# Kernel tuning notes

Measured on AMD Instinct MI355X. Metric: run time of the kernel, lower is better.

## Reference

```python
import jax, jax.numpy as jnp
import numpy as np

D_MODEL = 1024
NUM_HEADS = 16
HEAD_DIM = D_MODEL // NUM_HEADS  # 64
M_BITS = 32
B, N = 4, 2048


def setup_inputs() -> dict:
    key = jax.random.key(0)
    ks = jax.random.split(key, 6)
    s = 1.0 / np.sqrt(D_MODEL)
    se = 1.0 / np.sqrt(HEAD_DIM)
    return {
        "x": jax.random.normal(ks[0], (B, N, D_MODEL), dtype=jnp.float32),
        "Wq": jax.random.normal(ks[1], (D_MODEL, D_MODEL), dtype=jnp.float32) * s,
        "Wk": jax.random.normal(ks[2], (D_MODEL, D_MODEL), dtype=jnp.float32) * s,
        "Wv": jax.random.normal(ks[3], (D_MODEL, D_MODEL), dtype=jnp.float32) * s,
        # per-head witness (bit) encoders: project head_dim -> m_bits
        "W_enc": jax.random.normal(ks[4], (NUM_HEADS, HEAD_DIM, M_BITS), dtype=jnp.float32) * se,
        "Wo": jax.random.normal(ks[5], (D_MODEL, D_MODEL), dtype=jnp.float32) * s,
    }


def reference(x, Wq, Wk, Wv, W_enc, Wo):
    Bsz, Nq, _ = x.shape
    # QKV projections (nn.Linear, no bias): y = x @ W^T
    Q = x @ Wq.T
    K = x @ Wk.T  # self-attention: context = x
    V = x @ Wv.T
    # split heads: [B, N, H, hd]
    Qh = Q.reshape(Bsz, Nq, NUM_HEADS, HEAD_DIM)
    Kh = K.reshape(Bsz, Nq, NUM_HEADS, HEAD_DIM)
    Vh = V.reshape(Bsz, Nq, NUM_HEADS, HEAD_DIM)
    # witness encodings: soft-bit (tanh of random-hyperplane projections), m_bits << head_dim feature space
    q_enc = jnp.tanh(jnp.einsum("bnhd,hdm->bnhm", Qh, W_enc))
    k_enc = jnp.tanh(jnp.einsum("bnhd,hdm->bnhm", Kh, W_enc))
    # witness similarity scores over m_bits instead of full head_dim
    scale = 1.0 / np.sqrt(M_BITS)
    scores = jnp.einsum("bnhm,bkhm->bhnk", q_enc, k_enc) * scale  # [B,H,N,N]
    attn = jax.nn.softmax(scores, axis=-1)
    out = jnp.einsum("bhnk,bkhd->bnhd", attn, Vh).reshape(Bsz, Nq, D_MODEL)
    return out @ Wo.T
```

## Files before the change

### kernel.cpp

```cpp
#include <hip/hip_runtime.h>

typedef unsigned short u16;
typedef unsigned int u32;

typedef __bf16 bfrag __attribute__((ext_vector_type(8)));
typedef float f32x4 __attribute__((ext_vector_type(4)));
typedef float f32x16 __attribute__((ext_vector_type(16)));

__device__ __forceinline__ float b2f(u16 h) {
    u32 u = ((u32)h) << 16;
    return __builtin_bit_cast(float, u);
}
__device__ __forceinline__ u16 f2b(float f) {
    u32 u = __builtin_bit_cast(u32, f);
    u += 0x7fffu + ((u >> 16) & 1u);
    return (u16)(u >> 16);
}
__device__ __forceinline__ u32 packt(float lo, float hi) {
    return (__builtin_bit_cast(u32, lo) >> 16) | (__builtin_bit_cast(u32, hi) & 0xffff0000u);
}

#if defined(__has_builtin)
#if __has_builtin(__builtin_amdgcn_exp2f)
#define EXP2(x) __builtin_amdgcn_exp2f(x)
#endif
#endif
#ifndef EXP2
#define EXP2(x) exp2f(x)
#endif

#if defined(__has_builtin)
#if __has_builtin(__builtin_amdgcn_global_load_lds)
#define HAS_GLL 1
#endif
#endif
#ifndef HAS_GLL
#define HAS_GLL 0
#endif

#if HAS_GLL
typedef __attribute__((address_space(1))) const u32 as1_u32;
typedef __attribute__((address_space(3))) u32 as3_u32;
__device__ __forceinline__ void gl_lds16(const u16* g, u16* l) {
    __builtin_amdgcn_global_load_lds((as1_u32*)g, (as3_u32*)l, 16, 0, 0);
}
#endif

#if defined(__has_builtin)
#if __has_builtin(__builtin_amdgcn_permlane32_swap)
#define HAS_PLS 1
#endif
#endif
#ifndef HAS_PLS
#define HAS_PLS 0
#endif

__device__ __forceinline__ void plswap(u32 a, u32 b, u32& o0, u32& o1) {
#if HAS_PLS
    auto r = __builtin_amdgcn_permlane32_swap((int)a, (int)b, false, false);
    o0 = (u32)r[0];
    o1 = (u32)r[1];
#else
    int idx = ((int)(threadIdx.x & 63) ^ 32) << 2;
    u32 ca = (u32)__builtin_amdgcn_ds_bpermute(idx, (int)a);
    u32 cb = (u32)__builtin_amdgcn_ds_bpermute(idx, (int)b);
    bool hi = (threadIdx.x & 63) >= 32;
    o0 = hi ? cb : a;
    o1 = hi ? b : ca;
#endif
}

#define BATCH 4
#define SEQ   2048
#define DM    1024
#define NH    16
#define HD    64
#define MB    32
#define STOK  (BATCH * SEQ)
#define QKVW  (3 * DM)

#define QSCALE 0.25503524337503433f
#define TWOLOG2E 2.8853900817779268f

__device__ __forceinline__ void storeC(u16* C, size_t idx, float v)   { C[idx] = f2b(v); }
__device__ __forceinline__ void storeC(float* C, size_t idx, float v) { C[idx] = v; }

__global__ __launch_bounds__(256) void cvt_f32_bf16(
    const float* __restrict__ s, u16* __restrict__ d, int n8)
{
    int i = blockIdx.x * 256 + threadIdx.x;
    if (i >= n8) return;
    const float4* sp = (const float4*)s + (size_t)i * 2;
    float4 a = sp[0], b = sp[1];
    u16 t[8] = { f2b(a.x), f2b(a.y), f2b(a.z), f2b(a.w),
                 f2b(b.x), f2b(b.y), f2b(b.z), f2b(b.w) };
    ((uint4*)d)[i] = *(uint4*)t;
}

__global__ __launch_bounds__(256) void cvt3_f32_bf16(
    const float* __restrict__ a, const float* __restrict__ b,
    const float* __restrict__ c, u16* __restrict__ d, int n8)
{
    const float* s = (blockIdx.y == 0) ? a : ((blockIdx.y == 1) ? b : c);
    u16* dd = d + (size_t)blockIdx.y * n8 * 8;
    int i = blockIdx.x * 256 + threadIdx.x;
    if (i >= n8) return;
    const float4* sp = (const float4*)s + (size_t)i * 2;
    float4 x = sp[0], y = sp[1];
    u16 t[8] = { f2b(x.x), f2b(x.y), f2b(x.z), f2b(x.w),
                 f2b(y.x), f2b(y.y), f2b(y.z), f2b(y.w) };
    ((uint4*)dd)[i] = *(uint4*)t;
}

template <int TBM, typename TC>
__global__ __launch_bounds__(256) void gemm_bt(
    const u16* __restrict__ A, const u16* __restrict__ Bt, TC* __restrict__ C,
    int M, int Nc, int K)
{
    constexpr int FI = TBM / 32;
    __shared__ alignas(16) u16 As[TBM * 32];
    __shared__ alignas(16) u16 Bs[128 * 32];

    const int tid  = threadIdx.x;
    const int wave = tid >> 6;
    const int lane = tid & 63;
    const int quad = lane >> 4;
    const int lrow = lane & 15;
    const int bm = blockIdx.y * TBM;
    const int bn = blockIdx.x * 128;
    const int wm = (wave & 1) * (TBM / 2);
    const int wn = (wave >> 1) * 64;

    f32x4 acc[FI][4] = {};

    for (int k0 = 0; k0 < K; k0 += 32) {
#if HAS_GLL
        for (int p = 0; p < TBM / 64; ++p) {
            int cbase = wave * TBM + p * 64;
            int cme   = cbase + lane;
            int row = cme >> 2, col = (cme & 3) * 8;
            gl_lds16(&A[(size_t)(bm + row) * K + k0 + col], &As[(size_t)cbase * 8]);
        }
        for (int p = 0; p < 2; ++p) {
            int cbase = wave * 128 + p * 64;
            int cme   = cbase + lane;
            int row = cme >> 2, col = (cme & 3) * 8;
            gl_lds16(&Bt[(size_t)(bn + row) * K + k0 + col], &Bs[(size_t)cbase * 8]);
        }
#else
        for (int p = 0; p < TBM / 64; ++p) {
            int idx = p * 256 + tid, row = idx >> 2, col = (idx & 3) * 8;
            *(uint4*)&As[row * 32 + col] = *(const uint4*)&A[(size_t)(bm + row) * K + k0 + col];
        }
        for (int p = 0; p < 2; ++p) {
            int idx = p * 256 + tid, row = idx >> 2, col = (idx & 3) * 8;
            *(uint4*)&Bs[row * 32 + col] = *(const uint4*)&Bt[(size_t)(bn + row) * K + k0 + col];
        }
#endif
        __syncthreads();

        bfrag af[FI], bfv[4];
        for (int i = 0; i < FI; ++i)
            af[i] = *(const bfrag*)&As[(wm + i * 16 + lrow) * 32 + quad * 8];
        for (int j = 0; j < 4; ++j)
            bfv[j] = *(const bfrag*)&Bs[(wn + j * 16 + lrow) * 32 + quad * 8];

        for (int i = 0; i < FI; ++i)
            for (int j = 0; j < 4; ++j)
                acc[i][j] = __builtin_amdgcn_mfma_f32_16x16x32_bf16(af[i], bfv[j], acc[i][j], 0, 0, 0);
        __syncthreads();
    }

    for (int i = 0; i < FI; ++i)
        for (int j = 0; j < 4; ++j)
            for (int r = 0; r < 4; ++r) {
                int row = bm + wm + i * 16 + quad * 4 + r;
                int col = bn + wn + j * 16 + lrow;
                storeC(C, (size_t)row * Nc + col, acc[i][j][r]);
            }
}

__global__ __launch_bounds__(256) void encode_mfma(
    const u16* __restrict__ QKV, const float* __restrict__ Wenc,
    u16* __restrict__ qe, u16* __restrict__ ke)
{
    const int nt = blockIdx.x;
    const int bh = blockIdx.y;
    const int b = bh >> 4, h = bh & 15;
    const int tid = threadIdx.x;
    const int wave = tid >> 6, lane = tid & 63, quad = lane >> 4, lrow = lane & 15;

    __shared__ alignas(16) u16 Wh[32 * 72];
    __shared__ alignas(16) u16 Wl[32 * 72];
    __shared__ alignas(16) u16 Xt[128 * 72];

    for (int p = 0; p < 8; ++p) {
        int d = p * 8 + (tid >> 5);
        int m = tid & 31;
        float w = Wenc[(size_t)h * (HD * MB) + d * MB + m];
        u16 hi = f2b(w);
        u16 lo = f2b(w - b2f(hi));
        Wh[m * 72 + d] = hi;
        Wl[m * 72 + d] = lo;
    }
    __syncthreads();

    bfrag bhf[2][2], blf[2][2];
    for (int n2 = 0; n2 < 2; ++n2)
        for (int kc = 0; kc < 2; ++kc) {
            bhf[n2][kc] = *(const bfrag*)&Wh[(n2 * 16 + lrow) * 72 + kc * 32 + quad * 8];
            blf[n2][kc] = *(const bfrag*)&Wl[(n2 * 16 + lrow) * 72 + kc * 32 + quad * 8];
        }

    const f32x4 zero = {0.f, 0.f, 0.f, 0.f};
    for (int src = 0; src < 2; ++src) {
        __syncthreads();
        const u16* base = QKV + (size_t)(b * SEQ + nt * 128) * QKVW + src * DM + h * HD;
        for (int p = 0; p < 4; ++p) {
            int idx = p * 256 + tid;
            int row = idx >> 3, cc = idx & 7;
            *(uint4*)&Xt[row * 72 + cc * 8] = *(const uint4*)&base[(size_t)row * QKVW + cc * 8];
        }
        __syncthreads();

        u16* dst = (src ? ke : qe) + ((size_t)bh * SEQ + (size_t)nt * 128) * MB;
        for (int i = 0; i < 2; ++i) {
            bfrag af[2];
            for (int kc = 0; kc < 2; ++kc)
                af[kc] = *(const bfrag*)&Xt[(wave * 32 + i * 16 + lrow) * 72 + kc * 32 + quad * 8];
            for (int n2 = 0; n2 < 2; ++n2) {
                f32x4 acc = zero;
                for (int kc = 0; kc < 2; ++kc) {
                    acc = __builtin_amdgcn_mfma_f32_16x16x32_bf16(af[kc], bhf[n2][kc], acc, 0, 0, 0);
                    acc = __builtin_amdgcn_mfma_f32_16x16x32_bf16(af[kc], blf[n2][kc], acc, 0, 0, 0);
                }
                for (int r = 0; r < 4; ++r) {
                    float e = EXP2(acc[r] * TWOLOG2E);
                    float t = 1.f - 2.f / (e + 1.f);
                    if (!src) t *= QSCALE;
                    int tok = wave * 32 + i * 16 + quad * 4 + r;
                    dst[(size_t)tok * MB + n2 * 16 + lrow] = f2b(t);
                }
            }
        }
    }
}

__global__ __launch_bounds__(256) void transpose_v(
    const u16* __restrict__ QKV, u16* __restrict__ Vt)
{
    const int nt = blockIdx.x, h = blockIdx.y, b = blockIdx.z;
    __shared__ alignas(16) u16 tile[64][72];
    const int tid = threadIdx.x;

    for (int p = 0; p < 2; ++p) {
        int idx = p * 256 + tid;
        int t  = idx >> 3;
        int dc = (idx & 7) * 8;
        *(uint4*)&tile[t][dc] =
            *(const uint4*)&QKV[(size_t)(b * SEQ + nt * 64 + t) * QKVW + 2 * DM + h * HD + dc];
    }
    __syncthreads();
    for (int p = 0; p < 2; ++p) {
        int idx = p * 256 + tid;
        int d  = idx >> 3;
        int tc = (idx & 7) * 8;
        u16 tmp[8];
        for (int j = 0; j < 8; ++j) tmp[j] = tile[tc + j][d];
        *(uint4*)&Vt[(size_t)((b * NH + h) * HD + d) * SEQ + nt * 64 + tc] = *(uint4*)tmp;
    }
}

__global__ __launch_bounds__(256, 3) void flash_attn(
    const u16* __restrict__ qe,
    const u16* __restrict__ ke,
    const u16* __restrict__ Vt,
    u16* __restrict__ AO)
{
    const int h = blockIdx.x, b = blockIdx.y, qt = blockIdx.z;
    const int tid  = threadIdx.x;
    const int wave = tid >> 6;
    const int lane = tid & 63;
    const int r31  = lane & 31;
    const int hi   = lane >> 5;

    __shared__ alignas(16) u16 Kt[2][64 * 32];
    __shared__ alignas(16) u16 Vtile[2][64 * 64];

    const size_t bhh = (size_t)(b * NH + h);
    const u16* keb = ke + bhh * SEQ * MB;
    const u16* qeb = qe + bhh * SEQ * MB;
    const u16* vtb = Vt + bhh * HD * SEQ;

    const int q0w = qt * 128 + wave * 32;

    const int klr = tid >> 2;
    const int ksl = tid & 3;
    const u16* ksrc = keb + (size_t)klr * MB + ((ksl ^ (klr & 3)) * 8);
    const int d0 = wave * 8 + (lane >> 3);
    const int c0 = lane & 7;
    const int g0 = (c0 ^ (d0 & 7)) * 8;
    const u16* vsrc0 = vtb + (size_t)d0 * SEQ + g0;
    const u16* vsrc1 = vtb + (size_t)(d0 + 32) * SEQ + g0;

#if HAS_GLL
    gl_lds16(ksrc,  Kt[0] + wave * 512);
    gl_lds16(vsrc0, Vtile[0] + wave * 512);
    gl_lds16(vsrc1, Vtile[0] + 2048 + wave * 512);
#else
    *(uint4*)&Kt[0][klr * 32 + ksl * 8] = *(const uint4*)ksrc;
    *(uint4*)&Vtile[0][d0 * 64 + c0 * 8] = *(const uint4*)vsrc0;
    *(uint4*)&Vtile[0][(d0 + 32) * 64 + c0 * 8] = *(const uint4*)vsrc1;
#endif
    ksrc += 64 * MB;
    vsrc0 += 64;
    vsrc1 += 64;

    bfrag qf[2];
    {
        const u16* qrow = qeb + (size_t)(q0w + r31) * MB;
        qf[0] = *(const bfrag*)&qrow[hi * 8];
        qf[1] = *(const bfrag*)&qrow[16 + hi * 8];
    }

    const bfrag ones = __builtin_bit_cast(bfrag,
        (uint4){0x3f803f80u, 0x3f803f80u, 0x3f803f80u, 0x3f803f80u});
    const f32x16 zero16 = {};

    f32x16 Oa[2] = {};
    f32x16 den32 = {};
    const int ksw = r31 & 3;
    const int vsw = r31 & 7;

    for (int c = 0; c < 32; ++c) {
        const int cur = c & 1, nxt = cur ^ 1;
        __syncthreads();

        if (c + 1 < 32) {
#if HAS_GLL
            gl_lds16(ksrc,  Kt[nxt] + wave * 512);
            gl_lds16(vsrc0, Vtile[nxt] + wave * 512);
            gl_lds16(vsrc1, Vtile[nxt] + 2048 + wave * 512);
#else
            *(uint4*)&Kt[nxt][klr * 32 + ksl * 8] = *(const uint4*)ksrc;
            *(uint4*)&Vtile[nxt][d0 * 64 + c0 * 8] = *(const uint4*)vsrc0;
            *(uint4*)&Vtile[nxt][(d0 + 32) * 64 + c0 * 8] = *(const uint4*)vsrc1;
#endif
            ksrc += 64 * MB;
            vsrc0 += 64;
            vsrc1 += 64;
        }

        const u16* KtC = Kt[cur];
        const u16* VtC = Vtile[cur];

        bfrag kf[2][2];
        for (int kt = 0; kt < 2; ++kt) {
            const u16* krow = &KtC[(kt * 32 + r31) * 32];
            kf[kt][0] = *(const bfrag*)&krow[((hi    ) ^ ksw) * 8];
            kf[kt][1] = *(const bfrag*)&krow[((2 + hi) ^ ksw) * 8];
        }

        bfrag pf[2][2];
        for (int kt = 0; kt < 2; ++kt) {
            __builtin_amdgcn_s_setprio(1);
            f32x16 St = __builtin_amdgcn_mfma_f32_32x32x16_bf16(kf[kt][0], qf[0], zero16, 0, 0, 0);
            St = __builtin_amdgcn_mfma_f32_32x32x16_bf16(kf[kt][1], qf[1], St, 0, 0, 0);
            __builtin_amdgcn_s_setprio(0);
            for (int kc = 0; kc < 2; ++kc) {
                float e0 = EXP2(St[8 * kc + 0]);
                float e1 = EXP2(St[8 * kc + 1]);
                float e2 = EXP2(St[8 * kc + 2]);
                float e3 = EXP2(St[8 * kc + 3]);
                float e4 = EXP2(St[8 * kc + 4]);
                float e5 = EXP2(St[8 * kc + 5]);
                float e6 = EXP2(St[8 * kc + 6]);
                float e7 = EXP2(St[8 * kc + 7]);
                u32 A0 = packt(e0, e1), A1 = packt(e2, e3);
                u32 B0 = packt(e4, e5), B1 = packt(e6, e7);
                u32 w0, w1, w2, w3;
                plswap(A0, B0, w0, w2);
                plswap(A1, B1, w1, w3);
                uint4 words = { w0, w1, w2, w3 };
                pf[kt][kc] = __builtin_bit_cast(bfrag, words);
            }
        }

        __builtin_amdgcn_s_setprio(1);
        for (int kt = 0; kt < 2; ++kt)
            for (int kc = 0; kc < 2; ++kc)
                den32 = __builtin_amdgcn_mfma_f32_32x32x16_bf16(ones, pf[kt][kc], den32, 0, 0, 0);

        for (int dt = 0; dt < 2; ++dt) {
            const u16* vrow = &VtC[(dt * 32 + r31) * 64];
            for (int kt = 0; kt < 2; ++kt)
                for (int kc = 0; kc < 2; ++kc) {
                    bfrag vf = *(const bfrag*)&vrow[(((kt * 4 + kc * 2 + hi) ^ vsw) * 8)];
                    Oa[dt] = __builtin_amdgcn_mfma_f32_32x32x16_bf16(vf, pf[kt][kc], Oa[dt], 0, 0, 0);
                }
        }
        __builtin_amdgcn_s_setprio(0);
    }

    {
        float inv = 1.0f / den32[0];
        u16* aob = AO + (size_t)(b * SEQ + q0w + r31) * DM + h * HD;
        for (int dt = 0; dt < 2; ++dt)
            for (int g = 0; g < 4; ++g) {
                u16 t4[4] = { f2b(Oa[dt][g * 4 + 0] * inv),
                              f2b(Oa[dt][g * 4 + 1] * inv),
                              f2b(Oa[dt][g * 4 + 2] * inv),
                              f2b(Oa[dt][g * 4 + 3] * inv) };
                *(uint2*)&aob[dt * 32 + g * 8 + hi * 4] = *(uint2*)t4;
            }
    }
}

extern "C" void kernel_launch(void* const* d_in, const int* in_sizes, int n_in,
                              void* d_out, int out_size, void* d_ws, size_t ws_size,
                              hipStream_t stream) {
    const float* x    = (const float*)d_in[0];
    const float* Wq   = (const float*)d_in[1];
    const float* Wk   = (const float*)d_in[2];
    const float* Wv   = (const float*)d_in[3];
    const float* Wenc = (const float*)d_in[4];
    const float* Wo   = (const float*)d_in[5];
    float* out = (float*)d_out;

    const size_t MB1 = (size_t)1024 * 1024;
    char* ws = (char*)d_ws;
    u16* QKV = (u16*)(ws);
    u16* qe  = (u16*)(ws + 48 * MB1);
    u16* ke  = (u16*)(ws + 56 * MB1);
    u16* AO   = (u16*)(ws);
    u16* Wo_b = (u16*)(ws + 16 * MB1);

    u16* xb  = (u16*)d_out;
    u16* w3b = (u16*)((char*)d_out + 16 * MB1);
    u16* Vt  = (u16*)d_out;

    cvt_f32_bf16<<<dim3(STOK * DM / 8 / 256), 256, 0, stream>>>(x, xb, STOK * DM / 8);
    cvt3_f32_bf16<<<dim3(DM * DM / 8 / 256, 3), 256, 0, stream>>>(Wq, Wk, Wv, w3b, DM * DM / 8);

    gemm_bt<128, u16><<<dim3(QKVW / 128, STOK / 128), 256, 0, stream>>>(xb, w3b, QKV, STOK, QKVW, DM);

    encode_mfma<<<dim3(SEQ / 128, BATCH * NH), 256, 0, stream>>>(QKV, Wenc, qe, ke);
    transpose_v<<<dim3(SEQ / 64, NH, BATCH), 256, 0, stream>>>(QKV, Vt);
    cvt_f32_bf16<<<dim3(DM * DM / 8 / 256), 256, 0, stream>>>(Wo, Wo_b, DM * DM / 8);

    flash_attn<<<dim3(NH, BATCH, SEQ / 128), 256, 0, stream>>>(qe, ke, Vt, AO);

    gemm_bt<64, float><<<dim3(DM / 128, STOK / 64), 256, 0, stream>>>(AO, Wo_b, out, STOK, DM, DM);
}
```

Measured before the change: 298.7 us.

## Fold W_enc into Q/K weights and fuse encode and V transpose into GEMM epilogues

```diff
diff --git a/kernel.cpp b/kernel.cpp
--- a/kernel.cpp
+++ b/kernel.cpp
@@ -77,7 +77,6 @@
 #define HD    64
 #define MB    32
 #define STOK  (BATCH * SEQ)
-#define QKVW  (3 * DM)
 
 #define QSCALE 0.25503524337503433f
 #define TWOLOG2E 2.8853900817779268f
@@ -97,19 +96,34 @@
     ((uint4*)d)[i] = *(uint4*)t;
 }
 
-__global__ __launch_bounds__(256) void cvt3_f32_bf16(
-    const float* __restrict__ a, const float* __restrict__ b,
-    const float* __restrict__ c, u16* __restrict__ d, int n8)
+__global__ __launch_bounds__(256) void build_cqk(
+    const float* __restrict__ Wq, const float* __restrict__ Wk,
+    const float* __restrict__ Wenc, u16* __restrict__ CqkT)
 {
-    const float* s = (blockIdx.y == 0) ? a : ((blockIdx.y == 1) ? b : c);
-    u16* dd = d + (size_t)blockIdx.y * n8 * 8;
-    int i = blockIdx.x * 256 + threadIdx.x;
-    if (i >= n8) return;
-    const float4* sp = (const float4*)s + (size_t)i * 2;
-    float4 x = sp[0], y = sp[1];
-    u16 t[8] = { f2b(x.x), f2b(x.y), f2b(x.z), f2b(x.w),
-                 f2b(y.x), f2b(y.y), f2b(y.z), f2b(y.w) };
-    ((uint4*)dd)[i] = *(uint4*)t;
+    const int dblk = blockIdx.x;
+    const int qk   = blockIdx.y >> 4;
+    const int h    = blockIdx.y & 15;
+    const float* W = qk ? Wk : Wq;
+    __shared__ float we[64][32];
+    const int tid = threadIdx.x;
+
+    for (int p = 0; p < 8; ++p) {
+        int idx = p * 256 + tid;
+        we[idx >> 5][idx & 31] = Wenc[(size_t)h * (HD * MB) + idx];
+    }
+    __syncthreads();
+
+    const int mh = tid >> 7;
+    const int d  = dblk * 128 + (tid & 127);
+    float acc[16] = {};
+    for (int dh = 0; dh < 64; ++dh) {
+        float w = W[(size_t)(h * 64 + dh) * DM + d];
+        for (int m = 0; m < 16; ++m)
+            acc[m] += w * we[dh][mh * 16 + m];
+    }
+    u16* dst = CqkT + (size_t)(qk * 512 + h * 32 + mh * 16) * DM + d;
+    for (int m = 0; m < 16; ++m)
+        dst[(size_t)m * DM] = f2b(acc[m]);
 }
 
 template <int TBM, typename TC>
@@ -180,95 +194,131 @@
             }
 }
 
-__global__ __launch_bounds__(256) void encode_mfma(
-    const u16* __restrict__ QKV, const float* __restrict__ Wenc,
+__global__ __launch_bounds__(256) void gemm_enc(
+    const u16* __restrict__ A, const u16* __restrict__ Bt,
     u16* __restrict__ qe, u16* __restrict__ ke)
 {
-    const int nt = blockIdx.x;
-    const int bh = blockIdx.y;
-    const int b = bh >> 4, h = bh & 15;
-    const int tid = threadIdx.x;
-    const int wave = tid >> 6, lane = tid & 63, quad = lane >> 4, lrow = lane & 15;
-
-    __shared__ alignas(16) u16 Wh[32 * 72];
-    __shared__ alignas(16) u16 Wl[32 * 72];
-    __shared__ alignas(16) u16 Xt[128 * 72];
-
-    for (int p = 0; p < 8; ++p) {
-        int d = p * 8 + (tid >> 5);
-        int m = tid & 31;
-        float w = Wenc[(size_t)h * (HD * MB) + d * MB + m];
-        u16 hi = f2b(w);
-        u16 lo = f2b(w - b2f(hi));
-        Wh[m * 72 + d] = hi;
-        Wl[m * 72 + d] = lo;
-    }
-    __syncthreads();
-
-    bfrag bhf[2][2], blf[2][2];
-    for (int n2 = 0; n2 < 2; ++n2)
-        for (int kc = 0; kc < 2; ++kc) {
-            bhf[n2][kc] = *(const bfrag*)&Wh[(n2 * 16 + lrow) * 72 + kc * 32 + quad * 8];
-            blf[n2][kc] = *(const bfrag*)&Wl[(n2 * 16 + lrow) * 72 + kc * 32 + quad * 8];
-        }
-
-    const f32x4 zero = {0.f, 0.f, 0.f, 0.f};
-    for (int src = 0; src < 2; ++src) {
-        __syncthreads();
-        const u16* base = QKV + (size_t)(b * SEQ + nt * 128) * QKVW + src * DM + h * HD;
-        for (int p = 0; p < 4; ++p) {
-            int idx = p * 256 + tid;
-            int row = idx >> 3, cc = idx & 7;
-            *(uint4*)&Xt[row * 72 + cc * 8] = *(const uint4*)&base[(size_t)row * QKVW + cc * 8];
-        }
-        __syncthreads();
-
-        u16* dst = (src ? ke : qe) + ((size_t)bh * SEQ + (size_t)nt * 128) * MB;
-        for (int i = 0; i < 2; ++i) {
-            bfrag af[2];
-            for (int kc = 0; kc < 2; ++kc)
-                af[kc] = *(const bfrag*)&Xt[(wave * 32 + i * 16 + lrow) * 72 + kc * 32 + quad * 8];
-            for (int n2 = 0; n2 < 2; ++n2) {
-                f32x4 acc = zero;
-                for (int kc = 0; kc < 2; ++kc) {
-                    acc = __builtin_amdgcn_mfma_f32_16x16x32_bf16(af[kc], bhf[n2][kc], acc, 0, 0, 0);
-                    acc = __builtin_amdgcn_mfma_f32_16x16x32_bf16(af[kc], blf[n2][kc], acc, 0, 0, 0);
-                }
-                for (int r = 0; r < 4; ++r) {
-                    float e = EXP2(acc[r] * TWOLOG2E);
-                    float t = 1.f - 2.f / (e + 1.f);
-                    if (!src) t *= QSCALE;
-                    int tok = wave * 32 + i * 16 + quad * 4 + r;
-                    dst[(size_t)tok * MB + n2 * 16 + lrow] = f2b(t);
-                }
+    __shared__ alignas(16) u16 As[128 * 32];
+    __shared__ alignas(16) u16 Bs[128 * 32];
+
+    const int tid  = threadIdx.x;
+    const int wave = tid >> 6;
+    const int lane = tid & 63;
+    const int quad = lane >> 4;
+    const int lrow = lane & 15;
+    const int bm = blockIdx.y * 128;
+    const int bn = blockIdx.x * 128;
+    const int wm = (wave & 1) * 64;
+    const int wn = (wave >> 1) * 64;
+
+    f32x4 acc[4][4] = {};
+
+    for (int k0 = 0; k0 < DM; k0 += 32) {
+#if HAS_GLL
+        for (int p = 0; p < 2; ++p) {
+            int cbase = wave * 128 + p * 64;
+            int cme   = cbase + lane;
+            int row = cme >> 2, col = (cme & 3) * 8;
+            gl_lds16(&A[(size_t)(bm + row) * DM + k0 + col], &As[(size_t)cbase * 8]);
+            gl_lds16(&Bt[(size_t)(bn + row) * DM + k0 + col], &Bs[(size_t)cbase * 8]);
+        }
+#else
+        for (int p = 0; p < 2; ++p) {
+            int idx = p * 256 + tid, row = idx >> 2, col = (idx & 3) * 8;
+            *(uint4*)&As[row * 32 + col] = *(const uint4*)&A[(size_t)(bm + row) * DM + k0 + col];
+            *(uint4*)&Bs[row * 32 + col] = *(const uint4*)&Bt[(size_t)(bn + row) * DM + k0 + col];
+        }
+#endif
+        __syncthreads();
+
+        bfrag af[4], bfv[4];
+        for (int i = 0; i < 4; ++i)
+            af[i] = *(const bfrag*)&As[(wm + i * 16 + lrow) * 32 + quad * 8];
+        for (int j = 0; j < 4; ++j)
+            bfv[j] = *(const bfrag*)&Bs[(wn + j * 16 + lrow) * 32 + quad * 8];
+
+        for (int i = 0; i < 4; ++i)
+            for (int j = 0; j < 4; ++j)
+                acc[i][j] = __builtin_amdgcn_mfma_f32_16x16x32_bf16(af[i], bfv[j], acc[i][j], 0, 0, 0);
+        __syncthreads();
+    }
+
+    for (int i = 0; i < 4; ++i)
+        for (int j = 0; j < 4; ++j) {
+            int col = bn + wn + j * 16 + lrow;
+            int hh = (col >> 5) & 15;
+            int mm = col & 31;
+            u16* dst = (col < 512) ? qe : ke;
+            float qs = (col < 512) ? QSCALE : 1.0f;
+            for (int r = 0; r < 4; ++r) {
+                int row = bm + wm + i * 16 + quad * 4 + r;
+                int bb = row >> 11, nn = row & 2047;
+                float e = EXP2(acc[i][j][r] * TWOLOG2E);
+                float t = (1.f - 2.f / (e + 1.f)) * qs;
+                dst[((size_t)(bb * NH + hh) * SEQ + nn) * MB + mm] = f2b(t);
             }
         }
-    }
-}
-
-__global__ __launch_bounds__(256) void transpose_v(
-    const u16* __restrict__ QKV, u16* __restrict__ Vt)
+}
+
+__global__ __launch_bounds__(256) void gemm_vt(
+    const u16* __restrict__ A, const u16* __restrict__ Bt,
+    u16* __restrict__ Vt)
 {
-    const int nt = blockIdx.x, h = blockIdx.y, b = blockIdx.z;
-    __shared__ alignas(16) u16 tile[64][72];
-    const int tid = threadIdx.x;
-
-    for (int p = 0; p < 2; ++p) {
-        int idx = p * 256 + tid;
-        int t  = idx >> 3;
-        int dc = (idx & 7) * 8;
-        *(uint4*)&tile[t][dc] =
-            *(const uint4*)&QKV[(size_t)(b * SEQ + nt * 64 + t) * QKVW + 2 * DM + h * HD + dc];
-    }
-    __syncthreads();
-    for (int p = 0; p < 2; ++p) {
-        int idx = p * 256 + tid;
-        int d  = idx >> 3;
-        int tc = (idx & 7) * 8;
-        u16 tmp[8];
-        for (int j = 0; j < 8; ++j) tmp[j] = tile[tc + j][d];
-        *(uint4*)&Vt[(size_t)((b * NH + h) * HD + d) * SEQ + nt * 64 + tc] = *(uint4*)tmp;
-    }
+    __shared__ alignas(16) u16 As[128 * 32];
+    __shared__ alignas(16) u16 Bs[128 * 32];
+
+    const int tid  = threadIdx.x;
+    const int wave = tid >> 6;
+    const int lane = tid & 63;
+    const int quad = lane >> 4;
+    const int lrow = lane & 15;
+    const int bm = blockIdx.y * 128;
+    const int bn = blockIdx.x * 128;
+    const int wm = (wave & 1) * 64;
+    const int wn = (wave >> 1) * 64;
+
+    f32x4 acc[4][4] = {};
+
+    for (int k0 = 0; k0 < DM; k0 += 32) {
+#if HAS_GLL
+        for (int p = 0; p < 2; ++p) {
+            int cbase = wave * 128 + p * 64;
+            int cme   = cbase + lane;
+            int row = cme >> 2, col = (cme & 3) * 8;
+            gl_lds16(&A[(size_t)(bm + row) * DM + k0 + col], &As[(size_t)cbase * 8]);
+            gl_lds16(&Bt[(size_t)(bn + row) * DM + k0 + col], &Bs[(size_t)cbase * 8]);
+        }
+#else
+        for (int p = 0; p < 2; ++p) {
+            int idx = p * 256 + tid, row = idx >> 2, col = (idx & 3) * 8;
+            *(uint4*)&As[row * 32 + col] = *(const uint4*)&A[(size_t)(bm + row) * DM + k0 + col];
+            *(uint4*)&Bs[row * 32 + col] = *(const uint4*)&Bt[(size_t)(bn + row) * DM + k0 + col];
+        }
+#endif
+        __syncthreads();
+
+        bfrag af[4], bfv[4];
+        for (int i = 0; i < 4; ++i)
+            af[i] = *(const bfrag*)&As[(wm + i * 16 + lrow) * 32 + quad * 8];
+        for (int j = 0; j < 4; ++j)
+            bfv[j] = *(const bfrag*)&Bs[(wn + j * 16 + lrow) * 32 + quad * 8];
+
+        for (int i = 0; i < 4; ++i)
+            for (int j = 0; j < 4; ++j)
+                acc[i][j] = __builtin_amdgcn_mfma_f32_16x16x32_bf16(af[i], bfv[j], acc[i][j], 0, 0, 0);
+        __syncthreads();
+    }
+
+    for (int i = 0; i < 4; ++i)
+        for (int j = 0; j < 4; ++j) {
+            int col = bn + wn + j * 16 + lrow;
+            int hh = col >> 6, dd = col & 63;
+            int row0 = bm + wm + i * 16 + quad * 4;
+            int bb = row0 >> 11, nn = row0 & 2047;
+            u16 t4[4] = { f2b(acc[i][j][0]), f2b(acc[i][j][1]),
+                          f2b(acc[i][j][2]), f2b(acc[i][j][3]) };
+            *(uint2*)&Vt[((size_t)(bb * NH + hh) * HD + dd) * SEQ + nn] = *(uint2*)t4;
+        }
 }
 
 __global__ __launch_bounds__(256, 3) void flash_attn(
@@ -429,24 +479,23 @@
 
     const size_t MB1 = (size_t)1024 * 1024;
     char* ws = (char*)d_ws;
-    u16* QKV = (u16*)(ws);
-    u16* qe  = (u16*)(ws + 48 * MB1);
-    u16* ke  = (u16*)(ws + 56 * MB1);
     u16* AO   = (u16*)(ws);
     u16* Wo_b = (u16*)(ws + 16 * MB1);
+    u16* cqkT = (u16*)(ws + 18 * MB1);
+    u16* Vt   = (u16*)(ws + 24 * MB1);
+    u16* qe   = (u16*)(ws + 48 * MB1);
+    u16* ke   = (u16*)(ws + 56 * MB1);
 
     u16* xb  = (u16*)d_out;
-    u16* w3b = (u16*)((char*)d_out + 16 * MB1);
-    u16* Vt  = (u16*)d_out;
+    u16* wvb = (u16*)((char*)d_out + 16 * MB1);
 
     cvt_f32_bf16<<<dim3(STOK * DM / 8 / 256), 256, 0, stream>>>(x, xb, STOK * DM / 8);
-    cvt3_f32_bf16<<<dim3(DM * DM / 8 / 256, 3), 256, 0, stream>>>(Wq, Wk, Wv, w3b, DM * DM / 8);
-
-    gemm_bt<128, u16><<<dim3(QKVW / 128, STOK / 128), 256, 0, stream>>>(xb, w3b, QKV, STOK, QKVW, DM);
-
-    encode_mfma<<<dim3(SEQ / 128, BATCH * NH), 256, 0, stream>>>(QKV, Wenc, qe, ke);
-    transpose_v<<<dim3(SEQ / 64, NH, BATCH), 256, 0, stream>>>(QKV, Vt);
+    cvt_f32_bf16<<<dim3(DM * DM / 8 / 256), 256, 0, stream>>>(Wv, wvb, DM * DM / 8);
     cvt_f32_bf16<<<dim3(DM * DM / 8 / 256), 256, 0, stream>>>(Wo, Wo_b, DM * DM / 8);
+    build_cqk<<<dim3(8, 32), 256, 0, stream>>>(Wq, Wk, Wenc, cqkT);
+
+    gemm_enc<<<dim3(DM / 128, STOK / 128), 256, 0, stream>>>(xb, cqkT, qe, ke);
+    gemm_vt<<<dim3(DM / 128, STOK / 128), 256, 0, stream>>>(xb, wvb, Vt);
 
     flash_attn<<<dim3(NH, BATCH, SEQ / 128), 256, 0, stream>>>(qe, ke, Vt, AO);
 
```

Measured after the change: 271.7 us. 9.0% less time.
